# Optimization experiments

Measured on AMD Instinct MI355X. Metric: run time of the kernel, lower is better.

## Reference

```python
import jax, jax.numpy as jnp
import numpy as np

EPS = 1e-7  # K.epsilon()
NUM_ROUTING = 3


def squash(v, axis=-1):
    sq = jnp.sum(jnp.square(v), axis=axis, keepdims=True)
    return sq / (1.0 + sq) * (v / jnp.sqrt(sq + EPS))


def setup_inputs() -> dict:
    key = jax.random.key(0)
    k1, k2 = jax.random.split(key)
    B, NI, DI = 256, 1152, 8   # batch, input_num_capsule, input_dim_vector
    NJ, DJ = 10, 16            # num_capsule, dim_vector
    u = jax.random.normal(k1, (B, NI, DI), dtype=jnp.float32)
    W = jax.random.normal(k2, (NJ, NI, DJ, DI), dtype=jnp.float32) * 0.1
    return {"u": u, "W": W}


def reference(u, W):
    # u_hat[b,j,i,d] = sum_k u[b,i,k] * W[j,i,d,k]  (replaces tile + batch_dot)
    u_hat = jnp.einsum('bik,jidk->bjid', u, W)
    B, NJ, NI, _ = u_hat.shape
    b_ij = jnp.zeros((B, NJ, NI), dtype=u_hat.dtype)
    v_j = None
    for _ in range(NUM_ROUTING):
        c_ij = jax.nn.softmax(b_ij, axis=1)            # softmax over output capsules (dim=1)
        s_j = jnp.einsum('bji,bjid->bjd', c_ij, u_hat)  # weighted sum over input capsules
        v_j = squash(s_j)                               # (B, NJ, DJ)
        b_ij = b_ij + jnp.einsum('bjd,bjid->bji', v_j, u_hat)  # agreement update
    return v_j
```

## Files before the change

kernel.cpp:

```cpp
#include <hip/hip_runtime.h>
#include <math.h>

#define BB   256
#define NI   1152
#define DI   8
#define NJ   10
#define DJ   16
#define NCHUNK 18
#define CHUNK  64
#define BG     32
#define NBG    8
#define GRID_MAIN (NJ * NCHUNK * NBG)
#define BG2   8
#define GRID_BSA (8 * NCHUNK * (32 / BG2))
#define CTP2 68

typedef _Float16 half2_t __attribute__((ext_vector_type(2)));
typedef _Float16 half4_t __attribute__((ext_vector_type(4)));
typedef _Float16 half8_t __attribute__((ext_vector_type(8)));
typedef float    f32x4   __attribute__((ext_vector_type(4)));

template <int CTRL>
__device__ __forceinline__ float dpp_add(float x) {
    int xi = __float_as_int(x);
    int yi = __builtin_amdgcn_update_dpp(0, xi, CTRL, 0xF, 0xF, true);
    return x + __int_as_float(yi);
}

__device__ __forceinline__ float dot16(half8_t w, half8_t uu) {
    half2_t w0 = {w[0], w[1]}, w1 = {w[2], w[3]}, w2 = {w[4], w[5]}, w3 = {w[6], w[7]};
    half2_t a0 = {uu[0], uu[1]}, a1 = {uu[2], uu[3]}, a2 = {uu[4], uu[5]}, a3 = {uu[6], uu[7]};
    float acc = __builtin_amdgcn_fdot2(w0, a0, 0.f, false);
    acc = __builtin_amdgcn_fdot2(w1, a1, acc, false);
    acc = __builtin_amdgcn_fdot2(w2, a2, acc, false);
    acc = __builtin_amdgcn_fdot2(w3, a3, acc, false);
    return acc;
}

struct Ctx {
    int j, chunk, bg, i0, b0, tid, il, dq, lane, w, g, xcd, local;
};

__device__ __forceinline__ Ctx make_ctx(int bid, int tid) {
    Ctx c;
    c.xcd = bid & 7; c.local = bid >> 3;
    int gx = c.xcd * (GRID_MAIN / 8) + c.local;
    c.j = gx % NJ; int r = gx / NJ;
    c.chunk = r % NCHUNK; c.bg = r / NCHUNK;
    c.i0 = c.chunk * CHUNK; c.b0 = c.bg * BG;
    c.tid = tid; c.il = tid >> 2; c.dq = tid & 3;
    c.lane = tid & 63; c.w = tid >> 6; c.g = (c.lane >> 4) & 3;
    return c;
}

__device__ __forceinline__ void loadWf(const _Float16* __restrict__ W16, const Ctx& cx,
                                       half8_t* Wf) {
    int drow = cx.lane & 15, ksub = cx.lane >> 4;
#pragma unroll
    for (int qq = 0; qq < 4; ++qq) {
        int i = cx.i0 + cx.w * 16 + qq * 4 + ksub;
        Wf[qq] = *(const half8_t*)(W16 + (((size_t)cx.j * NI + i) * DJ + drow) * DI);
    }
}

__global__ __launch_bounds__(256) void k_cvt(const float* __restrict__ uf,
                                             const float* __restrict__ Wf,
                                             _Float16* __restrict__ u16,
                                             _Float16* __restrict__ W16) {
    const int nu4 = (BB * NI * DI) / 4;
    int base = (blockIdx.x * 256 + threadIdx.x) * 4;
    if (base < nu4) {
#pragma unroll
        for (int t = 0; t < 4; ++t) {
            float4 v = ((const float4*)uf)[base + t];
            half4_t h = {(_Float16)v.x, (_Float16)v.y, (_Float16)v.z, (_Float16)v.w};
            ((half4_t*)u16)[base + t] = h;
        }
    } else {
        int k = base - nu4;
#pragma unroll
        for (int t = 0; t < 4; ++t) {
            float4 v = ((const float4*)Wf)[k + t];
            half4_t h = {(_Float16)v.x, (_Float16)v.y, (_Float16)v.z, (_Float16)v.w};
            ((half4_t*)W16)[k + t] = h;
        }
    }
}

__global__ __launch_bounds__(256) void k_A0m(const _Float16* __restrict__ u16,
                                             const _Float16* __restrict__ W16,
                                             float* __restrict__ spart) {
    __shared__ __align__(16) float sres2[2 * 4 * 16 * 17];
    Ctx cx = make_ctx(blockIdx.x, threadIdx.x);
    half8_t Wf[4];
    loadWf(W16, cx, Wf);
    int l = cx.lane, w = cx.w;
    int drow = l & 15, ksub = l >> 4;

    half8_t au[2][4];
#pragma unroll
    for (int h = 0; h < 2; ++h) {
        int b = cx.b0 + h * 16 + drow;
#pragma unroll
        for (int qq = 0; qq < 4; ++qq) {
            int il = w * 16 + qq * 4 + ksub;
            au[h][qq] = *(const half8_t*)(u16 + ((size_t)b * NI + cx.i0 + il) * DI);
        }
    }
#pragma unroll
    for (int h = 0; h < 2; ++h) {
        f32x4 acc0 = {0.f, 0.f, 0.f, 0.f};
        f32x4 acc1 = {0.f, 0.f, 0.f, 0.f};
        acc0 = __builtin_amdgcn_mfma_f32_16x16x32_f16(au[h][0], Wf[0], acc0, 0, 0, 0);
        acc1 = __builtin_amdgcn_mfma_f32_16x16x32_f16(au[h][1], Wf[1], acc1, 0, 0, 0);
        acc0 = __builtin_amdgcn_mfma_f32_16x16x32_f16(au[h][2], Wf[2], acc0, 0, 0, 0);
        acc1 = __builtin_amdgcn_mfma_f32_16x16x32_f16(au[h][3], Wf[3], acc1, 0, 0, 0);
        f32x4 acc = acc0 + acc1;
#pragma unroll
        for (int r = 0; r < 4; ++r)
            sres2[((h * 4 + w) * 16 + ksub * 4 + r) * 17 + drow] = acc[r];
    }
    __syncthreads();
#pragma unroll
    for (int p = 0; p < 2; ++p) {
        int idx = p * 256 + cx.tid;
        int d = idx & 15, brow = (idx >> 4) & 15, h = idx >> 8;
        float s = 0.f;
#pragma unroll
        for (int w2 = 0; w2 < 4; ++w2)
            s += sres2[((h * 4 + w2) * 16 + brow) * 17 + d];
        s *= 0.1f;
        spart[(((size_t)cx.chunk * BB + cx.b0 + h * 16 + brow) * NJ + cx.j) * DJ + d] = s;
    }
}

template <int ITER>
__global__ __launch_bounds__(256) void k_BSA(const _Float16* __restrict__ u16,
                                             const _Float16* __restrict__ W16,
                                             float* __restrict__ spart,
                                             float* __restrict__ vbuf) {
    __shared__ __align__(16) float     vsm[BG2 * NJ * DJ];
    __shared__ __align__(16) _Float16  dtile[BG2 * NJ * CHUNK];
    __shared__ __align__(16) _Float16  ctile[NJ * BG2 * CTP2];
    __shared__ __align__(16) float     sres[NJ * 4 * BG2 * 17];

    int xcd = blockIdx.x & 7, local = blockIdx.x >> 3;
    int chunk = local % NCHUNK;
    int bgl   = local / NCHUNK;
    int b0 = xcd * 32 + bgl * BG2;
    int i0 = chunk * CHUNK;
    int tid = threadIdx.x;
    int lane = tid & 63, w = tid >> 6;
    int il = tid >> 2, dq = tid & 3;
    int drow = lane & 15, ksub = lane >> 4;
    bool brow_ok = drow < BG2;

    half8_t pu[BG2];
#pragma unroll
    for (int b8 = 0; b8 < BG2; ++b8)
        pu[b8] = *(const half8_t*)(u16 + ((size_t)(b0 + b8) * NI + i0 + il) * DI);
    half8_t au0[4];
#pragma unroll
    for (int qq = 0; qq < 4; ++qq) {
        int ili = w * 16 + qq * 4 + ksub;
        au0[qq] = brow_ok
            ? *(const half8_t*)(u16 + ((size_t)(b0 + drow) * NI + i0 + ili) * DI)
            : (half8_t){0, 0, 0, 0, 0, 0, 0, 0};
    }
    half8_t Wh[3][4];
#pragma unroll
    for (int jj = 0; jj < 2; ++jj) {
        const half8_t* wp = (const half8_t*)(W16 +
            (((size_t)jj * NI + i0 + il) * DJ + dq * 4) * DI);
#pragma unroll
        for (int q = 0; q < 4; ++q) Wh[jj][q] = wp[q];
    }

#pragma unroll
    for (int p = 0; p < 2; ++p) {
        int slot = p * 256 + tid;
        if (slot < BG2 * NJ * 4) {
            int b8 = slot / 40, rem = slot - b8 * 40;
            int j = rem >> 2, dq2 = rem & 3;
            int b = b0 + b8;
            float4 s4 = {0.f, 0.f, 0.f, 0.f};
#pragma unroll
            for (int ch = 0; ch < NCHUNK; ++ch) {
                float4 t = *(const float4*)&spart[(((size_t)ch * BB + b) * NJ + j) * DJ + dq2 * 4];
                s4.x += t.x; s4.y += t.y; s4.z += t.z; s4.w += t.w;
            }
            float sq = s4.x * s4.x + s4.y * s4.y + s4.z * s4.z + s4.w * s4.w;
            sq = dpp_add<0x0B1>(sq);
            sq = dpp_add<0x04E>(sq);
            float scale = (sq / (1.f + sq)) / sqrtf(sq + 1e-7f);
            float4 vv; vv.x = s4.x * scale; vv.y = s4.y * scale;
            vv.z = s4.z * scale; vv.w = s4.w * scale;
            size_t va = ((size_t)b * NJ + j) * DJ + dq2 * 4;
            if (ITER == 0) {
                if (chunk == 0) *(float4*)&vbuf[va] = vv;
            } else {
                float4 v0 = *(const float4*)&vbuf[va];
                vv.x += v0.x; vv.y += v0.y; vv.z += v0.z; vv.w += v0.w;
            }
            *(float4*)&vsm[(b8 * NJ + j) * DJ + dq2 * 4] = vv;
        }
    }
    __syncthreads();

#pragma unroll
    for (int j = 0; j < NJ; ++j) {
        if (j + 2 < NJ) {
            const half8_t* wp = (const half8_t*)(W16 +
                (((size_t)(j + 2) * NI + i0 + il) * DJ + dq * 4) * DI);
#pragma unroll
            for (int q = 0; q < 4; ++q) Wh[(j + 2) % 3][q] = wp[q];
        }
        float pj[BG2];
#pragma unroll
        for (int b8 = 0; b8 < BG2; ++b8) {
            float4 vv = *(const float4*)&vsm[(b8 * NJ + j) * DJ + dq * 4];
            float p = vv.x * dot16(Wh[j % 3][0], pu[b8]);
            p = fmaf(vv.y, dot16(Wh[j % 3][1], pu[b8]), p);
            p = fmaf(vv.z, dot16(Wh[j % 3][2], pu[b8]), p);
            p = fmaf(vv.w, dot16(Wh[j % 3][3], pu[b8]), p);
            p = dpp_add<0x0B1>(p);
            p = dpp_add<0x04E>(p);
            pj[b8] = p;
        }
        if (dq == 0) {
#pragma unroll
            for (int b8 = 0; b8 < BG2; ++b8)
                dtile[(b8 * NJ + j) * CHUNK + il] = (_Float16)pj[b8];
        }
    }

    half8_t Wf[3][4];
#pragma unroll
    for (int jj = 0; jj < 2; ++jj) {
#pragma unroll
        for (int qq = 0; qq < 4; ++qq) {
            int i = i0 + w * 16 + qq * 4 + ksub;
            Wf[jj][qq] = *(const half8_t*)(W16 + (((size_t)jj * NI + i) * DJ + drow) * DI);
        }
    }
    __syncthreads();

#pragma unroll
    for (int p = 0; p < 2; ++p) {
        int pair = p * 256 + tid;
        int b8 = pair >> 6, i = pair & 63;
        float x[NJ]; float ssum = 0.f;
#pragma unroll
        for (int j = 0; j < NJ; ++j) {
            x[j] = __expf((float)dtile[(b8 * NJ + j) * CHUNK + i]);
            ssum += x[j];
        }
        float rs = 1.f / ssum;
#pragma unroll
        for (int j = 0; j < NJ; ++j)
            ctile[(j * BG2 + b8) * CTP2 + i] = (_Float16)(x[j] * rs);
    }
    __syncthreads();

#pragma unroll
    for (int j = 0; j < NJ; ++j) {
        if (j + 2 < NJ) {
#pragma unroll
            for (int qq = 0; qq < 4; ++qq) {
                int i = i0 + w * 16 + qq * 4 + ksub;
                Wf[(j + 2) % 3][qq] =
                    *(const half8_t*)(W16 + (((size_t)(j + 2) * NI + i) * DJ + drow) * DI);
            }
        }
        half8_t av[4];
#pragma unroll
        for (int qq = 0; qq < 4; ++qq) {
            int ili = w * 16 + qq * 4 + ksub;
            _Float16 ch = brow_ok ? ctile[(j * BG2 + drow) * CTP2 + ili] : (_Float16)0.f;
            half8_t cc = {ch, ch, ch, ch, ch, ch, ch, ch};
            av[qq] = au0[qq] * cc;
        }
        f32x4 acc0 = {0.f, 0.f, 0.f, 0.f};
        f32x4 acc1 = {0.f, 0.f, 0.f, 0.f};
        acc0 = __builtin_amdgcn_mfma_f32_16x16x32_f16(av[0], Wf[j % 3][0], acc0, 0, 0, 0);
        acc1 = __builtin_amdgcn_mfma_f32_16x16x32_f16(av[1], Wf[j % 3][1], acc1, 0, 0, 0);
        acc0 = __builtin_amdgcn_mfma_f32_16x16x32_f16(av[2], Wf[j % 3][2], acc0, 0, 0, 0);
        acc1 = __builtin_amdgcn_mfma_f32_16x16x32_f16(av[3], Wf[j % 3][3], acc1, 0, 0, 0);
        f32x4 acc = acc0 + acc1;
        if (ksub < 2) {
#pragma unroll
            for (int r = 0; r < 4; ++r)
                sres[((j * 4 + w) * BG2 + ksub * 4 + r) * 17 + drow] = acc[r];
        }
    }
    __syncthreads();
#pragma unroll
    for (int p = 0; p < 5; ++p) {
        int idx = p * 256 + tid;
        int d = idx & 15, brow2 = (idx >> 4) & 7, j = idx >> 7;
        float s = 0.f;
#pragma unroll
        for (int w2 = 0; w2 < 4; ++w2)
            s += sres[((j * 4 + w2) * BG2 + brow2) * 17 + d];
        spart[(((size_t)chunk * BB + b0 + brow2) * NJ + j) * DJ + d] = s;
    }
}

__global__ __launch_bounds__(256) void k_V(const float* __restrict__ spart,
                                           float* __restrict__ out) {
    int idx4 = blockIdx.x * 256 + threadIdx.x;
    float4 s4 = {0.f, 0.f, 0.f, 0.f};
#pragma unroll
    for (int ch = 0; ch < NCHUNK; ++ch) {
        float4 t = *(const float4*)&spart[(size_t)ch * (BB * NJ * DJ) + (size_t)idx4 * 4];
        s4.x += t.x; s4.y += t.y; s4.z += t.z; s4.w += t.w;
    }
    float sq = s4.x * s4.x + s4.y * s4.y + s4.z * s4.z + s4.w * s4.w;
    sq = dpp_add<0x0B1>(sq);
    sq = dpp_add<0x04E>(sq);
    float scale = (sq / (1.f + sq)) / sqrtf(sq + 1e-7f);
    float4 o; o.x = s4.x * scale; o.y = s4.y * scale;
    o.z = s4.z * scale; o.w = s4.w * scale;
    *(float4*)&out[(size_t)idx4 * 4] = o;
}

extern "C" void kernel_launch(void* const* d_in, const int* in_sizes, int n_in,
                              void* d_out, int out_size, void* d_ws, size_t ws_size,
                              hipStream_t stream) {
    const float* u = (const float*)d_in[0];
    const float* W = (const float*)d_in[1];
    float* out = (float*)d_out;

    float*     spart = (float*)d_ws;
    float*     vbuf  = spart + (size_t)NCHUNK * BB * NJ * DJ;
    _Float16*  u16   = (_Float16*)(vbuf + (size_t)BB * NJ * DJ);
    _Float16*  W16   = u16 + (size_t)BB * NI * DI;

    dim3 blk(256);
    const int GRID_CVT = ((BB * NI * DI) / 4 + (NJ * NI * DJ * DI) / 4) / (256 * 4);

    k_cvt<<<GRID_CVT, blk, 0, stream>>>(u, W, u16, W16);
    k_A0m<<<GRID_MAIN, blk, 0, stream>>>(u16, W16, spart);
    k_BSA<0><<<GRID_BSA, blk, 0, stream>>>(u16, W16, spart, vbuf);
    k_BSA<1><<<GRID_BSA, blk, 0, stream>>>(u16, W16, spart, vbuf);
    k_V<<<40, blk, 0, stream>>>(spart, out);
}
```

Measured before the change: 73.32 us.

## Split output-capsule loop across two half-blocks and ping-pong partial-sum buffers

k_BSA now launches 512 threads per block, and the two 256-thread halves handle even and odd output capsules. Each half runs five iterations of the agreement and MFMA loops instead of ten, which shortens each block's serial dependency chain. The partial-sum buffer becomes two buffers used alternately as input and output, so a block no longer overwrites sums that other blocks of the same launch may still be reading. The cost is more registers and shared-memory pressure per block, and the extra buffer uses more workspace.

```diff
diff --git a/kernel.cpp b/kernel.cpp
--- a/kernel.cpp
+++ b/kernel.cpp
@@ -135,9 +135,10 @@
 }
 
 template <int ITER>
-__global__ __launch_bounds__(256) void k_BSA(const _Float16* __restrict__ u16,
+__global__ __launch_bounds__(512) void k_BSA(const _Float16* __restrict__ u16,
                                              const _Float16* __restrict__ W16,
-                                             float* __restrict__ spart,
+                                             const float* __restrict__ sin,
+                                             float* __restrict__ sout,
                                              float* __restrict__ vbuf) {
     __shared__ __align__(16) float     vsm[BG2 * NJ * DJ];
     __shared__ __align__(16) _Float16  dtile[BG2 * NJ * CHUNK];
@@ -150,8 +151,10 @@
     int b0 = xcd * 32 + bgl * BG2;
     int i0 = chunk * CHUNK;
     int tid = threadIdx.x;
-    int lane = tid & 63, w = tid >> 6;
-    int il = tid >> 2, dq = tid & 3;
+    int jh = tid >> 8;
+    int half_tid = tid & 255;
+    int lane = tid & 63, w = (tid >> 6) & 3;
+    int il = half_tid >> 2, dq = tid & 3;
     int drow = lane & 15, ksub = lane >> 4;
     bool brow_ok = drow < BG2;
 
@@ -169,16 +172,16 @@
     }
     half8_t Wh[3][4];
 #pragma unroll
-    for (int jj = 0; jj < 2; ++jj) {
+    for (int it = 0; it < 2; ++it) {
+        int j = it * 2 + jh;
         const half8_t* wp = (const half8_t*)(W16 +
-            (((size_t)jj * NI + i0 + il) * DJ + dq * 4) * DI);
-#pragma unroll
-        for (int q = 0; q < 4; ++q) Wh[jj][q] = wp[q];
-    }
-
-#pragma unroll
-    for (int p = 0; p < 2; ++p) {
-        int slot = p * 256 + tid;
+            (((size_t)j * NI + i0 + il) * DJ + dq * 4) * DI);
+#pragma unroll
+        for (int q = 0; q < 4; ++q) Wh[it][q] = wp[q];
+    }
+
+    {
+        int slot = tid;
         if (slot < BG2 * NJ * 4) {
             int b8 = slot / 40, rem = slot - b8 * 40;
             int j = rem >> 2, dq2 = rem & 3;
@@ -186,7 +189,7 @@
             float4 s4 = {0.f, 0.f, 0.f, 0.f};
 #pragma unroll
             for (int ch = 0; ch < NCHUNK; ++ch) {
-                float4 t = *(const float4*)&spart[(((size_t)ch * BB + b) * NJ + j) * DJ + dq2 * 4];
+                float4 t = *(const float4*)&sin[(((size_t)ch * BB + b) * NJ + j) * DJ + dq2 * 4];
                 s4.x += t.x; s4.y += t.y; s4.z += t.z; s4.w += t.w;
             }
             float sq = s4.x * s4.x + s4.y * s4.y + s4.z * s4.z + s4.w * s4.w;
@@ -208,21 +211,22 @@
     __syncthreads();
 
 #pragma unroll
-    for (int j = 0; j < NJ; ++j) {
-        if (j + 2 < NJ) {
+    for (int it = 0; it < 5; ++it) {
+        int j = it * 2 + jh;
+        if (it + 2 < 5) {
             const half8_t* wp = (const half8_t*)(W16 +
-                (((size_t)(j + 2) * NI + i0 + il) * DJ + dq * 4) * DI);
-#pragma unroll
-            for (int q = 0; q < 4; ++q) Wh[(j + 2) % 3][q] = wp[q];
+                (((size_t)(j + 4) * NI + i0 + il) * DJ + dq * 4) * DI);
+#pragma unroll
+            for (int q = 0; q < 4; ++q) Wh[(it + 2) % 3][q] = wp[q];
         }
         float pj[BG2];
 #pragma unroll
         for (int b8 = 0; b8 < BG2; ++b8) {
             float4 vv = *(const float4*)&vsm[(b8 * NJ + j) * DJ + dq * 4];
-            float p = vv.x * dot16(Wh[j % 3][0], pu[b8]);
-            p = fmaf(vv.y, dot16(Wh[j % 3][1], pu[b8]), p);
-            p = fmaf(vv.z, dot16(Wh[j % 3][2], pu[b8]), p);
-            p = fmaf(vv.w, dot16(Wh[j % 3][3], pu[b8]), p);
+            float p = vv.x * dot16(Wh[it % 3][0], pu[b8]);
+            p = fmaf(vv.y, dot16(Wh[it % 3][1], pu[b8]), p);
+            p = fmaf(vv.z, dot16(Wh[it % 3][2], pu[b8]), p);
+            p = fmaf(vv.w, dot16(Wh[it % 3][3], pu[b8]), p);
             p = dpp_add<0x0B1>(p);
             p = dpp_add<0x04E>(p);
             pj[b8] = p;
@@ -236,19 +240,18 @@
 
     half8_t Wf[3][4];
 #pragma unroll
-    for (int jj = 0; jj < 2; ++jj) {
+    for (int it = 0; it < 2; ++it) {
+        int j = it * 2 + jh;
 #pragma unroll
         for (int qq = 0; qq < 4; ++qq) {
             int i = i0 + w * 16 + qq * 4 + ksub;
-            Wf[jj][qq] = *(const half8_t*)(W16 + (((size_t)jj * NI + i) * DJ + drow) * DI);
-        }
-    }
-    __syncthreads();
-
-#pragma unroll
-    for (int p = 0; p < 2; ++p) {
-        int pair = p * 256 + tid;
-        int b8 = pair >> 6, i = pair & 63;
+            Wf[it][qq] = *(const half8_t*)(W16 + (((size_t)j * NI + i) * DJ + drow) * DI);
+        }
+    }
+    __syncthreads();
+
+    {
+        int b8 = tid >> 6, i = tid & 63;
         float x[NJ]; float ssum = 0.f;
 #pragma unroll
         for (int j = 0; j < NJ; ++j) {
@@ -263,13 +266,14 @@
     __syncthreads();
 
 #pragma unroll
-    for (int j = 0; j < NJ; ++j) {
-        if (j + 2 < NJ) {
+    for (int it = 0; it < 5; ++it) {
+        int j = it * 2 + jh;
+        if (it + 2 < 5) {
 #pragma unroll
             for (int qq = 0; qq < 4; ++qq) {
                 int i = i0 + w * 16 + qq * 4 + ksub;
-                Wf[(j + 2) % 3][qq] =
-                    *(const half8_t*)(W16 + (((size_t)(j + 2) * NI + i) * DJ + drow) * DI);
+                Wf[(it + 2) % 3][qq] =
+                    *(const half8_t*)(W16 + (((size_t)(j + 4) * NI + i) * DJ + drow) * DI);
             }
         }
         half8_t av[4];
@@ -282,10 +286,10 @@
         }
         f32x4 acc0 = {0.f, 0.f, 0.f, 0.f};
         f32x4 acc1 = {0.f, 0.f, 0.f, 0.f};
-        acc0 = __builtin_amdgcn_mfma_f32_16x16x32_f16(av[0], Wf[j % 3][0], acc0, 0, 0, 0);
-        acc1 = __builtin_amdgcn_mfma_f32_16x16x32_f16(av[1], Wf[j % 3][1], acc1, 0, 0, 0);
-        acc0 = __builtin_amdgcn_mfma_f32_16x16x32_f16(av[2], Wf[j % 3][2], acc0, 0, 0, 0);
-        acc1 = __builtin_amdgcn_mfma_f32_16x16x32_f16(av[3], Wf[j % 3][3], acc1, 0, 0, 0);
+        acc0 = __builtin_amdgcn_mfma_f32_16x16x32_f16(av[0], Wf[it % 3][0], acc0, 0, 0, 0);
+        acc1 = __builtin_amdgcn_mfma_f32_16x16x32_f16(av[1], Wf[it % 3][1], acc1, 0, 0, 0);
+        acc0 = __builtin_amdgcn_mfma_f32_16x16x32_f16(av[2], Wf[it % 3][2], acc0, 0, 0, 0);
+        acc1 = __builtin_amdgcn_mfma_f32_16x16x32_f16(av[3], Wf[it % 3][3], acc1, 0, 0, 0);
         f32x4 acc = acc0 + acc1;
         if (ksub < 2) {
 #pragma unroll
@@ -295,14 +299,16 @@
     }
     __syncthreads();
 #pragma unroll
-    for (int p = 0; p < 5; ++p) {
-        int idx = p * 256 + tid;
-        int d = idx & 15, brow2 = (idx >> 4) & 7, j = idx >> 7;
-        float s = 0.f;
-#pragma unroll
-        for (int w2 = 0; w2 < 4; ++w2)
-            s += sres[((j * 4 + w2) * BG2 + brow2) * 17 + d];
-        spart[(((size_t)chunk * BB + b0 + brow2) * NJ + j) * DJ + d] = s;
+    for (int p = 0; p < 3; ++p) {
+        int idx = p * 512 + tid;
+        if (idx < NJ * BG2 * DJ) {
+            int d = idx & 15, brow2 = (idx >> 4) & 7, j = idx >> 7;
+            float s = 0.f;
+#pragma unroll
+            for (int w2 = 0; w2 < 4; ++w2)
+                s += sres[((j * 4 + w2) * BG2 + brow2) * 17 + d];
+            sout[(((size_t)chunk * BB + b0 + brow2) * NJ + j) * DJ + d] = s;
+        }
     }
 }
 
@@ -331,17 +337,19 @@
     const float* W = (const float*)d_in[1];
     float* out = (float*)d_out;
 
-    float*     spart = (float*)d_ws;
-    float*     vbuf  = spart + (size_t)NCHUNK * BB * NJ * DJ;
-    _Float16*  u16   = (_Float16*)(vbuf + (size_t)BB * NJ * DJ);
-    _Float16*  W16   = u16 + (size_t)BB * NI * DI;
+    const size_t SPART_N = (size_t)NCHUNK * BB * NJ * DJ;
+    float*     spartA = (float*)d_ws;
+    float*     spartB = spartA + SPART_N;
+    float*     vbuf   = spartB + SPART_N;
+    _Float16*  u16    = (_Float16*)(vbuf + (size_t)BB * NJ * DJ);
+    _Float16*  W16    = u16 + (size_t)BB * NI * DI;
 
     dim3 blk(256);
     const int GRID_CVT = ((BB * NI * DI) / 4 + (NJ * NI * DJ * DI) / 4) / (256 * 4);
 
     k_cvt<<<GRID_CVT, blk, 0, stream>>>(u, W, u16, W16);
-    k_A0m<<<GRID_MAIN, blk, 0, stream>>>(u16, W16, spart);
-    k_BSA<0><<<GRID_BSA, blk, 0, stream>>>(u16, W16, spart, vbuf);
-    k_BSA<1><<<GRID_BSA, blk, 0, stream>>>(u16, W16, spart, vbuf);
-    k_V<<<40, blk, 0, stream>>>(spart, out);
-}
+    k_A0m<<<GRID_MAIN, blk, 0, stream>>>(u16, W16, spartA);
+    k_BSA<0><<<GRID_BSA, dim3(512), 0, stream>>>(u16, W16, spartA, spartB, vbuf);
+    k_BSA<1><<<GRID_BSA, dim3(512), 0, stream>>>(u16, W16, spartB, spartA, vbuf);
+    k_V<<<40, blk, 0, stream>>>(spartA, out);
+}
```

Result: slower. 90.80 us (+23.8%).
